# Kernel tuning notes

Measured on AMD Instinct MI355X. Metric: run time of the kernel, lower is better.

Reference implementation:

```python
import jax, jax.numpy as jnp
import numpy as np

DIM, HEADS, HEAD_DIM, P = 256, 8, 64, 16
N = P * P          # 256 tokens
H2 = HEADS // 2    # heads in SDPA branch
SCALE = HEAD_DIM ** -0.5
BN_EPS = 1e-5


def _depthwise(x, w, kh, kw):
    # x: (b, DIM, P, P), w: (DIM, kh*kw) depthwise kernel -> same spatial size
    rhs = w.reshape(DIM, 1, kh, kw)
    return jax.lax.conv_general_dilated(
        x, rhs, window_strides=(1, 1),
        padding=((kh // 2, kh // 2), (kw // 2, kw // 2)),
        dimension_numbers=('NCHW', 'OIHW', 'NCHW'),
        feature_group_count=DIM)


def setup_inputs() -> dict:
    key = jax.random.key(0)
    ks = jax.random.split(key, 8)
    b = 128
    return {
        'x': jax.random.normal(ks[0], (b, N, DIM), jnp.float32),
        'bn_gamma': jax.random.uniform(ks[1], (DIM,), jnp.float32, 0.5, 1.5),
        'bn_beta': jax.random.normal(ks[2], (DIM,), jnp.float32) * 0.1,
        'bn_mean': jax.random.normal(ks[3], (DIM,), jnp.float32) * 0.1,
        'bn_var': jax.random.uniform(ks[4], (DIM,), jnp.float32, 0.5, 1.5),
        'w_qkv': jax.random.normal(ks[5], (DIM, 6), jnp.float32) * 0.1,
        'w_qs': jax.random.normal(ks[6], (DIM, 3), jnp.float32) * 0.1,
        'w_ks': jax.random.normal(ks[7], (DIM, 3), jnp.float32) * 0.1,
    }


def reference(x, bn_gamma, bn_beta, bn_mean, bn_var, w_qkv, w_qs, w_ks):
    b = x.shape[0]
    # raw contiguous view (b,n,d) -> (b,dim,p,p), as in the torch code
    xi = x.reshape(b, DIM, P, P)
    inv = jax.lax.rsqrt(bn_var + BN_EPS)
    xb = jax.nn.relu(((xi - bn_mean[None, :, None, None]) * (bn_gamma * inv)[None, :, None, None])
                     + bn_beta[None, :, None, None])
    # grouped 1x1 conv (groups=DIM, 6 out-channels per group)
    qkv = (xb[:, :, None, :, :] * w_qkv[None, :, :, None, None]).reshape(b, DIM * 6, P, P)
    # raw view (b, 6*dim, p, p) -> (b, n, 6*dim)
    qkv = qkv.reshape(b, N, 6 * DIM)
    q, k, v = jnp.split(qkv, 3, axis=-1)  # each (b, n, 2*dim)

    def to_heads(t):
        return t.reshape(b, N, HEADS, HEAD_DIM).transpose(0, 2, 1, 3)  # b h n d

    q, k, v = to_heads(q), to_heads(k), to_heads(v)
    q1, k1, v1 = q[:, :H2], k[:, :H2], v[:, :H2]
    # raw reshape (b, H2, n, head_dim) -> (b, dim, p, p)
    q2 = q[:, H2:].reshape(b, DIM, P, P)
    k2 = k[:, H2:].reshape(b, DIM, P, P)
    v2 = v[:, H2:].reshape(b, DIM, P, P)
    q2 = _depthwise(q2, w_qs, 1, 3)
    k2 = _depthwise(k2, w_ks, 3, 1)
    res2 = (q2 + k2 + v2).reshape(b, N, DIM)

    scores = jnp.einsum('bhid,bhjd->bhij', q1, k1) * SCALE
    attn = jax.nn.softmax(scores, axis=-1)
    out = jnp.einsum('bhij,bhjd->bhid', attn, v1)
    out = out.transpose(0, 2, 1, 3).reshape(b, N, H2 * HEAD_DIM)  # (b, n, dim)

    res = jnp.concatenate([out, res2], axis=2)  # (b, n, 2*dim)
    # AdaptiveAvgPool1d(dim) on length 2*dim == pairwise mean
    return res.reshape(b, N, DIM, 2).mean(axis=-1)
```

## Files before the change

kernel.cpp:

```cpp
#include <hip/hip_runtime.h>

typedef __bf16 bf16;
typedef __attribute__((ext_vector_type(8))) __bf16 bf16x8;
typedef __attribute__((ext_vector_type(4))) __bf16 bf16x4;
typedef __attribute__((ext_vector_type(2))) __bf16 bf16x2;
typedef __attribute__((ext_vector_type(4))) float floatx4;

#define MFMA16(a,b,c) __builtin_amdgcn_mfma_f32_16x16x32_bf16((a),(b),(c),0,0,0)

__device__ __forceinline__ float fast_exp2(float xv) {
#if __has_builtin(__builtin_amdgcn_exp2f)
  return __builtin_amdgcn_exp2f(xv);
#else
  return exp2f(xv);
#endif
}

__device__ __forceinline__ void ld8f(const bf16* p, float* dst) {
  bf16x8 v = *(const bf16x8*)p;
#pragma unroll
  for (int i = 0; i < 8; ++i) dst[i] = (float)v[i];
}

__global__ __launch_bounds__(512, 4) void fused_kernel(
    const float* __restrict__ x,
    const float* __restrict__ bn_gamma, const float* __restrict__ bn_beta,
    const float* __restrict__ bn_mean, const float* __restrict__ bn_var,
    const float* __restrict__ w_qkv, const float* __restrict__ w_qs,
    const float* __restrict__ w_ks,
    float* __restrict__ out)
{
  __shared__ __align__(16) char smem[49152];
  bf16 (*Abf)[72]    = (bf16(*)[72])smem;
  bf16 (*Vt)[64][40] = (bf16(*)[64][40])(smem + 36864);
  float* ckA = (float*)(smem + 47104);
  float* cvA = (float*)(smem + 48128);
  float* scT = (float*)(smem + 36864);
  float* bsT = (float*)(smem + 36864 + 1024);
  float* Lsh = (float*)(smem + 36864);

  const int t  = threadIdx.x;
  const int bb = blockIdx.x >> 2;
  const int h  = blockIdx.x & 3;

  if (t < 256) {
    float inv = rsqrtf(bn_var[t] + 1e-5f);
    float sc  = bn_gamma[t] * inv;
    scT[t] = sc;
    bsT[t] = bn_beta[t] - bn_mean[t] * sc;
    ckA[t] = w_qkv[t*6+2];
    cvA[t] = w_qkv[t*6+4];
  }
  __syncthreads();

  const float* xb = x + (size_t)bb * 65536 + h * 64;
  {
    const int rsub = t >> 4, ch = t & 15;
#pragma unroll
    for (int i2 = 0; i2 < 8; ++i2) {
      int n = i2*32 + rsub;
      float4 v = *(const float4*)(xb + (size_t)n*256 + ch*4);
      float sc = scT[n], bs = bsT[n];
      bf16x4 bv;
      bv.x = (bf16)fmaxf(fmaf(v.x, sc, bs), 0.f);
      bv.y = (bf16)fmaxf(fmaf(v.y, sc, bs), 0.f);
      bv.z = (bf16)fmaxf(fmaf(v.z, sc, bs), 0.f);
      bv.w = (bf16)fmaxf(fmaf(v.w, sc, bs), 0.f);
      *(bf16x4*)&Abf[n][ch*4] = bv;
    }
  }
  __syncthreads();

  {
    int j = t & 31, g = t >> 5;
    bf16x4 v = *(const bf16x4*)&Abf[j][g*4];
    Vt[0][g*4+0][j] = v.x; Vt[0][g*4+1][j] = v.y;
    Vt[0][g*4+2][j] = v.z; Vt[0][g*4+3][j] = v.w;
  }

  const int lane = t & 63;
  const int wid  = t >> 6;
  const int q    = lane >> 4;
  const int c    = lane & 15;
  const int R    = wid * 32;
  const bool hi  = (q >= 2);
  const int qa   = q & 1;
  const int srcA = ((qa*2)*16 + c) * 4;
  const int srcB = ((qa*2+1)*16 + c) * 4;

  float cqv[2];
  cqv[0] = w_qkv[(R + c)*6]      * 0.18033688f;
  cqv[1] = w_qkv[(R + 16 + c)*6] * 0.18033688f;

  floatx4 oacc[2][4];
  float lacc[2] = {0.f, 0.f};
#pragma unroll
  for (int it = 0; it < 2; ++it)
#pragma unroll
    for (int et = 0; et < 4; ++et)
      oacc[it][et] = (floatx4){0.f,0.f,0.f,0.f};

  for (int jt = 0; jt < 8; ++jt) {
    const int j0  = jt * 32;
    const int cur = jt & 1;
    __syncthreads();

    if (jt < 7) {
      int j = t & 31, g = t >> 5;
      bf16x4 v = *(const bf16x4*)&Abf[j0 + 32 + j][g*4];
      Vt[cur^1][g*4+0][j] = v.x; Vt[cur^1][g*4+1][j] = v.y;
      Vt[cur^1][g*4+2][j] = v.z; Vt[cur^1][g*4+3][j] = v.w;
    }

    bf16x8 aj00 = *(const bf16x8*)&Abf[j0 + c][8*q];
    bf16x8 aj01 = *(const bf16x8*)&Abf[j0 + c][32 + 8*q];
    bf16x8 aj10 = *(const bf16x8*)&Abf[j0 + 16 + c][8*q];
    bf16x8 aj11 = *(const bf16x8*)&Abf[j0 + 16 + c][32 + 8*q];
    floatx4 ckv0 = *(const floatx4*)&ckA[j0 + 4*q];
    floatx4 ckv1 = *(const floatx4*)&ckA[j0 + 16 + 4*q];
    floatx4 cvv0 = *(const floatx4*)&cvA[j0 + 4*q];
    floatx4 cvv1 = *(const floatx4*)&cvA[j0 + 16 + 4*q];

    unsigned int paU[2][4];
#pragma unroll
    for (int it = 0; it < 2; ++it) {
      const bf16* bp = &Abf[R + 16*it + c][0];
      bf16x8 bi0 = *(const bf16x8*)(bp + 8*q);
      bf16x8 bi1 = *(const bf16x8*)(bp + 32 + 8*q);
      floatx4 s0 = (floatx4){0.f,0.f,0.f,0.f};
      floatx4 s1 = (floatx4){0.f,0.f,0.f,0.f};
      s0 = MFMA16(aj00, bi0, s0); s0 = MFMA16(aj01, bi1, s0);
      s1 = MFMA16(aj10, bi0, s1); s1 = MFMA16(aj11, bi1, s1);
      float p0[4], p1[4];
#pragma unroll
      for (int r = 0; r < 4; ++r) {
        float e0v = fast_exp2(fminf(cqv[it]*ckv0[r]*s0[r], 80.f));
        float e1v = fast_exp2(fminf(cqv[it]*ckv1[r]*s1[r], 80.f));
        lacc[it] += e0v + e1v;
        p0[r] = e0v * cvv0[r];
        p1[r] = e1v * cvv1[r];
      }
      union { bf16x2 hh; unsigned int u; } pk00, pk01, pk10, pk11;
      pk00.hh = (bf16x2){(bf16)p0[0], (bf16)p0[1]};
      pk01.hh = (bf16x2){(bf16)p0[2], (bf16)p0[3]};
      pk10.hh = (bf16x2){(bf16)p1[0], (bf16)p1[1]};
      pk11.hh = (bf16x2){(bf16)p1[2], (bf16)p1[3]};
      unsigned int a0, a1;
      a0 = (unsigned)__builtin_amdgcn_ds_bpermute(srcA, (int)pk00.u);
      a1 = (unsigned)__builtin_amdgcn_ds_bpermute(srcA, (int)pk10.u);
      paU[it][0] = hi ? a1 : a0;
      a0 = (unsigned)__builtin_amdgcn_ds_bpermute(srcA, (int)pk01.u);
      a1 = (unsigned)__builtin_amdgcn_ds_bpermute(srcA, (int)pk11.u);
      paU[it][1] = hi ? a1 : a0;
      a0 = (unsigned)__builtin_amdgcn_ds_bpermute(srcB, (int)pk00.u);
      a1 = (unsigned)__builtin_amdgcn_ds_bpermute(srcB, (int)pk10.u);
      paU[it][2] = hi ? a1 : a0;
      a0 = (unsigned)__builtin_amdgcn_ds_bpermute(srcB, (int)pk01.u);
      a1 = (unsigned)__builtin_amdgcn_ds_bpermute(srcB, (int)pk11.u);
      paU[it][3] = hi ? a1 : a0;
    }

    union PAu { unsigned int u[4]; bf16x8 v; };
    PAu pa0, pa1;
#pragma unroll
    for (int k = 0; k < 4; ++k) { pa0.u[k] = paU[0][k]; pa1.u[k] = paU[1][k]; }

#pragma unroll
    for (int et = 0; et < 4; ++et) {
      bf16x8 vb = *(const bf16x8*)&Vt[cur][16*et + c][8*q];
      oacc[0][et] = MFMA16(pa0.v, vb, oacc[0][et]);
      oacc[1][et] = MFMA16(pa1.v, vb, oacc[1][et]);
    }
  }

  __syncthreads();

#pragma unroll
  for (int it = 0; it < 2; ++it) {
    float v = lacc[it];
    v += __shfl_xor(v, 16, 64);
    v += __shfl_xor(v, 32, 64);
    lacc[it] = v;
  }
  if (q == 0) {
    Lsh[R + c]      = lacc[0];
    Lsh[R + 16 + c] = lacc[1];
  }
  floatx4 l40 = *(const floatx4*)&Lsh[R + 4*q];
  floatx4 l41 = *(const floatx4*)&Lsh[R + 16 + 4*q];

  float* outA = out + ((size_t)bb*256)*256 + h*32;
#pragma unroll
  for (int it = 0; it < 2; ++it) {
    floatx4 l4 = it ? l41 : l40;
#pragma unroll
    for (int r = 0; r < 4; ++r) {
      float linv = 0.5f / l4[r];
      int n = R + 16*it + 4*q + r;
#pragma unroll
      for (int et = 0; et < 4; ++et) {
        float v = oacc[it][et][r];
        float v2 = v + __shfl_xor(v, 1, 64);
        if (!(lane & 1))
          outA[(size_t)n*256 + 8*et + (c>>1)] = v2 * linv;
      }
    }
  }

  {
    const int ci = t >> 3, sub = t & 7, qq = sub >> 1, uh = sub & 1;
    const int C  = h*64 + ci;
    const int a  = 4*ci + qq;
    const int e0 = 32*uh;

    float qs0 = w_qs[C*3+0], qs1 = w_qs[C*3+1], qs2 = w_qs[C*3+2];
    float ks0 = w_ks[C*3+0], ks1 = w_ks[C*3+1], ks2 = w_ks[C*3+2];
    float wq1a = w_qkv[a*6+1], wk1a = w_qkv[a*6+3], wv1a = w_qkv[a*6+5];
    float wcf = fmaf(ks1, wk1a, wv1a);

    float wmx = 0.f;
    if (uh) wmx = ks0 * wk1a;
    else if (qq > 0) wmx = ks0 * w_qkv[(a-1)*6+3];
    float wmh = ks0 * wk1a;
    float wpl = ks2 * wk1a;
    float wpx = 0.f;
    if (!uh) wpx = ks2 * wk1a;
    else if (qq < 3) wpx = ks2 * w_qkv[(a+1)*6+3];

    float Xc[32], Xl[16], Xr[16];
#pragma unroll
    for (int m = 0; m < 4; ++m) ld8f(&Abf[a][e0 + 8*m], &Xc[8*m]);
    if (uh) {
      ld8f(&Abf[a][16], &Xl[0]); ld8f(&Abf[a][24], &Xl[8]);
    } else if (qq > 0) {
      ld8f(&Abf[a-1][48], &Xl[0]); ld8f(&Abf[a-1][56], &Xl[8]);
    } else {
#pragma unroll
      for (int i = 0; i < 16; ++i) Xl[i] = 0.f;
    }
    if (!uh) {
      ld8f(&Abf[a][32], &Xr[0]); ld8f(&Abf[a][40], &Xr[8]);
    } else if (qq < 3) {
      ld8f(&Abf[a+1][0], &Xr[0]); ld8f(&Abf[a+1][8], &Xr[8]);
    } else {
#pragma unroll
      for (int i = 0; i < 16; ++i) Xr[i] = 0.f;
    }

    float res[16];
    float prev = 0.f;
#pragma unroll
    for (int k = 0; k < 32; ++k) {
      float fc = Xc[k];
      float qv = qs1 * fc;
      if (k & 15)         qv = fmaf(qs0, Xc[k-1], qv);
      if ((k & 15) != 15) qv = fmaf(qs2, Xc[k+1], qv);
      float acc = fmaf(wq1a, qv, wcf * fc);
      float tm = (k < 16) ? Xl[k]     : Xc[k-16];
      float wm = (k < 16) ? wmx       : wmh;
      acc = fmaf(wm, tm, acc);
      float tp = (k < 16) ? Xc[k+16]  : Xr[k-16];
      float wp = (k < 16) ? wpl       : wpx;
      acc = fmaf(wp, tp, acc);
      if (k & 1) res[k>>1] = 0.5f * (prev + acc);
      else       prev = acc;
    }

    float* outC = out + ((size_t)(bb*256 + C))*256 + 128 + 32*qq + 16*uh;
#pragma unroll
    for (int m = 0; m < 4; ++m) {
      float4 o4;
      o4.x = res[4*m]; o4.y = res[4*m+1]; o4.z = res[4*m+2]; o4.w = res[4*m+3];
      *(float4*)(outC + 4*m) = o4;
    }
  }
}

extern "C" void kernel_launch(void* const* d_in, const int* in_sizes, int n_in,
                              void* d_out, int out_size, void* d_ws, size_t ws_size,
                              hipStream_t stream) {
  (void)in_sizes; (void)n_in; (void)out_size; (void)d_ws; (void)ws_size;
  const float* x    = (const float*)d_in[0];
  const float* g    = (const float*)d_in[1];
  const float* be   = (const float*)d_in[2];
  const float* mn   = (const float*)d_in[3];
  const float* vr   = (const float*)d_in[4];
  const float* wqkv = (const float*)d_in[5];
  const float* wqs  = (const float*)d_in[6];
  const float* wks  = (const float*)d_in[7];
  float* out = (float*)d_out;

  fused_kernel<<<dim3(512), dim3(512), 0, stream>>>(x, g, be, mn, vr, wqkv, wqs, wks, out);
}
```

Baseline: 113.8 us.

## Precompute full scaled V-transpose in LDS to drop per-tile barriers

```diff
diff --git a/kernel.cpp b/kernel.cpp
--- a/kernel.cpp
+++ b/kernel.cpp
@@ -30,14 +30,13 @@
     const float* __restrict__ w_ks,
     float* __restrict__ out)
 {
-  __shared__ __align__(16) char smem[49152];
-  bf16 (*Abf)[72]    = (bf16(*)[72])smem;
-  bf16 (*Vt)[64][40] = (bf16(*)[64][40])(smem + 36864);
-  float* ckA = (float*)(smem + 47104);
-  float* cvA = (float*)(smem + 48128);
+  __shared__ __align__(16) char smem[72704];
+  bf16 (*Abf)[72]  = (bf16(*)[72])smem;
+  bf16 (*VtF)[264] = (bf16(*)[264])(smem + 36864);
+  float* ckA = (float*)(smem + 70656);
+  float* cvA = (float*)(smem + 71680);
   float* scT = (float*)(smem + 36864);
   float* bsT = (float*)(smem + 36864 + 1024);
-  float* Lsh = (float*)(smem + 36864);
 
   const int t  = threadIdx.x;
   const int bb = blockIdx.x >> 2;
@@ -72,11 +71,19 @@
   __syncthreads();
 
   {
-    int j = t & 31, g = t >> 5;
-    bf16x4 v = *(const bf16x4*)&Abf[j][g*4];
-    Vt[0][g*4+0][j] = v.x; Vt[0][g*4+1][j] = v.y;
-    Vt[0][g*4+2][j] = v.z; Vt[0][g*4+3][j] = v.w;
-  }
+    const int j32 = t & 31, g = t >> 5;
+#pragma unroll
+    for (int jt = 0; jt < 8; ++jt) {
+      int j = jt*32 + j32;
+      bf16x4 v = *(const bf16x4*)&Abf[j][g*4];
+      float cv = cvA[j];
+      VtF[g*4+0][j] = (bf16)((float)v.x * cv);
+      VtF[g*4+1][j] = (bf16)((float)v.y * cv);
+      VtF[g*4+2][j] = (bf16)((float)v.z * cv);
+      VtF[g*4+3][j] = (bf16)((float)v.w * cv);
+    }
+  }
+  __syncthreads();
 
   const int lane = t & 63;
   const int wid  = t >> 6;
@@ -92,6 +99,14 @@
   cqv[0] = w_qkv[(R + c)*6]      * 0.18033688f;
   cqv[1] = w_qkv[(R + 16 + c)*6] * 0.18033688f;
 
+  bf16x8 bi0[2], bi1[2];
+#pragma unroll
+  for (int it = 0; it < 2; ++it) {
+    const bf16* bp = &Abf[R + 16*it + c][0];
+    bi0[it] = *(const bf16x8*)(bp + 8*q);
+    bi1[it] = *(const bf16x8*)(bp + 32 + 8*q);
+  }
+
   floatx4 oacc[2][4];
   float lacc[2] = {0.f, 0.f};
 #pragma unroll
@@ -101,16 +116,7 @@
       oacc[it][et] = (floatx4){0.f,0.f,0.f,0.f};
 
   for (int jt = 0; jt < 8; ++jt) {
-    const int j0  = jt * 32;
-    const int cur = jt & 1;
-    __syncthreads();
-
-    if (jt < 7) {
-      int j = t & 31, g = t >> 5;
-      bf16x4 v = *(const bf16x4*)&Abf[j0 + 32 + j][g*4];
-      Vt[cur^1][g*4+0][j] = v.x; Vt[cur^1][g*4+1][j] = v.y;
-      Vt[cur^1][g*4+2][j] = v.z; Vt[cur^1][g*4+3][j] = v.w;
-    }
+    const int j0 = jt * 32;
 
     bf16x8 aj00 = *(const bf16x8*)&Abf[j0 + c][8*q];
     bf16x8 aj01 = *(const bf16x8*)&Abf[j0 + c][32 + 8*q];
@@ -118,27 +124,22 @@
     bf16x8 aj11 = *(const bf16x8*)&Abf[j0 + 16 + c][32 + 8*q];
     floatx4 ckv0 = *(const floatx4*)&ckA[j0 + 4*q];
     floatx4 ckv1 = *(const floatx4*)&ckA[j0 + 16 + 4*q];
-    floatx4 cvv0 = *(const floatx4*)&cvA[j0 + 4*q];
-    floatx4 cvv1 = *(const floatx4*)&cvA[j0 + 16 + 4*q];
 
     unsigned int paU[2][4];
 #pragma unroll
     for (int it = 0; it < 2; ++it) {
-      const bf16* bp = &Abf[R + 16*it + c][0];
-      bf16x8 bi0 = *(const bf16x8*)(bp + 8*q);
-      bf16x8 bi1 = *(const bf16x8*)(bp + 32 + 8*q);
       floatx4 s0 = (floatx4){0.f,0.f,0.f,0.f};
       floatx4 s1 = (floatx4){0.f,0.f,0.f,0.f};
-      s0 = MFMA16(aj00, bi0, s0); s0 = MFMA16(aj01, bi1, s0);
-      s1 = MFMA16(aj10, bi0, s1); s1 = MFMA16(aj11, bi1, s1);
+      s0 = MFMA16(aj00, bi0[it], s0); s0 = MFMA16(aj01, bi1[it], s0);
+      s1 = MFMA16(aj10, bi0[it], s1); s1 = MFMA16(aj11, bi1[it], s1);
       float p0[4], p1[4];
 #pragma unroll
       for (int r = 0; r < 4; ++r) {
         float e0v = fast_exp2(fminf(cqv[it]*ckv0[r]*s0[r], 80.f));
         float e1v = fast_exp2(fminf(cqv[it]*ckv1[r]*s1[r], 80.f));
         lacc[it] += e0v + e1v;
-        p0[r] = e0v * cvv0[r];
-        p1[r] = e1v * cvv1[r];
+        p0[r] = e0v;
+        p1[r] = e1v;
       }
       union { bf16x2 hh; unsigned int u; } pk00, pk01, pk10, pk11;
       pk00.hh = (bf16x2){(bf16)p0[0], (bf16)p0[1]};
@@ -167,13 +168,11 @@
 
 #pragma unroll
     for (int et = 0; et < 4; ++et) {
-      bf16x8 vb = *(const bf16x8*)&Vt[cur][16*et + c][8*q];
+      bf16x8 vb = *(const bf16x8*)&VtF[16*et + c][j0 + 8*q];
       oacc[0][et] = MFMA16(pa0.v, vb, oacc[0][et]);
       oacc[1][et] = MFMA16(pa1.v, vb, oacc[1][et]);
     }
   }
-
-  __syncthreads();
 
 #pragma unroll
   for (int it = 0; it < 2; ++it) {
@@ -182,20 +181,14 @@
     v += __shfl_xor(v, 32, 64);
     lacc[it] = v;
   }
-  if (q == 0) {
-    Lsh[R + c]      = lacc[0];
-    Lsh[R + 16 + c] = lacc[1];
-  }
-  floatx4 l40 = *(const floatx4*)&Lsh[R + 4*q];
-  floatx4 l41 = *(const floatx4*)&Lsh[R + 16 + 4*q];
 
   float* outA = out + ((size_t)bb*256)*256 + h*32;
 #pragma unroll
   for (int it = 0; it < 2; ++it) {
-    floatx4 l4 = it ? l41 : l40;
 #pragma unroll
     for (int r = 0; r < 4; ++r) {
-      float linv = 0.5f / l4[r];
+      float lsrc = __shfl(lacc[it], 4*q + r, 64);
+      float linv = 0.5f / lsrc;
       int n = R + 16*it + 4*q + r;
 #pragma unroll
       for (int et = 0; et < 4; ++et) {
```

New measurement: 109.9 us. 3.4% less time.
